# Kernel optimization log

Measured on AMD Instinct MI355X. Metric: run time of the kernel, lower is better.

The kernel has to match this reference:

```python
import jax, jax.numpy as jnp
import numpy as np

B, S, D, H, HG, W, DFF = 2, 4096, 1024, 16, 2, 128, 4096
NEG = -1e30  # stands in for -inf in the original masking (exp underflows to exactly 0)


def _chunk(x, w):
    # overlapping chunks of size 2w with hop w (tf.signal.frame equivalent)
    b, s, d = x.shape
    blocks = x.reshape(b, s // w, w, d)
    return jnp.concatenate([blocks[:, :-1], blocks[:, 1:]], axis=2)  # [b, s//w-1, 2w, d]


def _sliding_scores(q, k, w):
    # q,k: [BH, S, dh] (q pre-scaled). Returns banded scores [BH, S, 2w+1].
    bh, s, d = q.shape
    c = s // w - 1
    attn = jnp.einsum('bcxd,bcyd->bcxy', _chunk(q, w), _chunk(k, w))  # [bh,c,2w,2w]
    # pad one row then reshape: the skew trick from the source (_pad_and_transpose_last_two_dims)
    dca = jnp.pad(attn, ((0, 0), (0, 0), (0, 1), (0, 0))).reshape(bh, c, 2 * w, 2 * w + 1)
    up = jnp.concatenate([dca[:, :, :w, :w + 1], dca[:, -1:, w:, :w + 1]], axis=1)          # [bh,c+1,w,w+1]
    first = jnp.roll(dca, shift=(1, w), axis=(2, 3))[:, :1, :w, :w]                          # first-chunk lower triangle
    low = jnp.concatenate([first, dca[:, :, -(w + 1):-1, w + 1:]], axis=1)                   # [bh,c+1,w,w]
    return jnp.concatenate([low, up], axis=-1).reshape(bh, s, 2 * w + 1)


def _invalid_mask(s, w):
    # _mask_invalid_locations: mask band positions that fall outside [0, S)
    m = jnp.tril(jnp.ones((w, w + 1), jnp.float32))[::-1]
    m = jnp.pad(m, ((0, s - w), (0, w)))
    return (m + m[::-1, ::-1]) > 0  # [s, 2w+1]


def _sliding_value(p, v, w):
    # p: [BH, S, 2w+1] band probs, v: [BH, S, dh] -> [BH, S, dh]
    bh, s, kk = p.shape
    d = v.shape[-1]
    c = s // w
    cp = jnp.pad(p.reshape(bh, c, w, kk), ((0, 0), (0, 0), (0, 0), (0, w + 1)))
    # pad-and-diagonalize skew: row r shifted right by r -> aligns band with 3w value window
    cp = cp.reshape(bh, c, w * (3 * w + 2))[:, :, :-w].reshape(bh, c, w, 3 * w + 1)[:, :, :, :-1]
    pv = jnp.pad(v, ((0, 0), (w, w), (0, 0))).reshape(bh, c + 2, w, d)
    cv = jnp.concatenate([pv[:, :-2], pv[:, 1:-1], pv[:, 2:]], axis=2)  # [bh,c,3w,d]
    return jnp.einsum('bcwk,bckd->bcwd', cp, cv).reshape(bh, s, d)


def _layernorm(x, g, b):
    mu = jnp.mean(x, -1, keepdims=True)
    var = jnp.mean(jnp.square(x - mu), -1, keepdims=True)
    return (x - mu) * jax.lax.rsqrt(var + 1e-6) * g + b


def setup_inputs() -> dict:
    key = jax.random.key(0)
    ks = jax.random.split(key, 8)
    dense = lambda k, i, o: 0.02 * jax.random.normal(k, (i, o), jnp.float32)
    return {
        'x': jax.random.normal(ks[0], (B, S, D), jnp.float32),
        'mask': jnp.zeros((B, 1, 1, S), jnp.float32),
        'wq_k': dense(ks[1], D, D), 'wq_b': jnp.zeros((D,), jnp.float32),
        'wk_k': dense(ks[2], D, D), 'wk_b': jnp.zeros((D,), jnp.float32),
        'wv_k': dense(ks[3], D, D), 'wv_b': jnp.zeros((D,), jnp.float32),
        'wo_k': dense(ks[4], D, D), 'wo_b': jnp.zeros((D,), jnp.float32),
        'ffn_w1': dense(ks[5], D, DFF), 'ffn_b1': jnp.zeros((DFF,), jnp.float32),
        'ffn_w2': dense(ks[6], DFF, D), 'ffn_b2': jnp.zeros((D,), jnp.float32),
        'ln1_g': jnp.ones((D,), jnp.float32), 'ln1_b': jnp.zeros((D,), jnp.float32),
        'ln2_g': jnp.ones((D,), jnp.float32), 'ln2_b': jnp.zeros((D,), jnp.float32),
    }


def reference(x, mask, wq_k, wq_b, wk_k, wk_b, wv_k, wv_b, wo_k, wo_b,
              ffn_w1, ffn_b1, ffn_w2, ffn_b2, ln1_g, ln1_b, ln2_g, ln2_b):
    dh = D // H
    hl = H - HG
    split = lambda t: t.reshape(B, S, H, dh).transpose(0, 2, 1, 3)  # [B,H,S,dh]
    q, k, v = split(x @ wq_k + wq_b), split(x @ wk_k + wk_b), split(x @ wv_k + wv_b)
    scale = 1.0 / jnp.sqrt(jnp.float32(dh))
    # ---- local (sliding-window) heads ----
    ql = (q[:, :hl] * scale).reshape(B * hl, S, dh)
    kl = k[:, :hl].reshape(B * hl, S, dh)
    vl = v[:, :hl].reshape(B * hl, S, dh)
    scores = _sliding_scores(ql, kl, W)
    scores = jnp.where(_invalid_mask(S, W)[None], NEG, scores)
    out_l = _sliding_value(jax.nn.softmax(scores, axis=-1), vl, W).reshape(B, hl, S, dh)
    # ---- global heads (full attention, graph_mask=None branch) ----
    logits = jnp.einsum('bhqd,bhkd->bhqk', q[:, hl:], k[:, hl:]) * scale + mask * (-1000.0)
    out_g = jnp.einsum('bhqk,bhkd->bhqd', jax.nn.softmax(logits, axis=-1), v[:, hl:])
    # ---- merge heads, output proj, residual + LN, FFN (leaky_relu alpha=0.2 = tf default) ----
    attn = jnp.concatenate([out_l, out_g], axis=1).transpose(0, 2, 1, 3).reshape(B, S, D)
    out1 = _layernorm(x + attn @ wo_k + wo_b, ln1_g, ln1_b)
    h = jax.nn.leaky_relu(out1 @ ffn_w1 + ffn_b1, negative_slope=0.2)
    return _layernorm(out1 + h @ ffn_w2 + ffn_b2, ln2_g, ln2_b)
```

## Files before the change

### kernel.cpp

```cpp
#include <hip/hip_runtime.h>
#include <hip/hip_bf16.h>

typedef unsigned short u16;
typedef unsigned int u32;
typedef __attribute__((ext_vector_type(8))) short short8;
typedef __attribute__((ext_vector_type(8))) unsigned short ushort8v;
typedef __attribute__((ext_vector_type(4))) unsigned short ushort4v;
typedef __attribute__((ext_vector_type(4))) float f32x4;

static constexpr int B_ = 2, S_ = 4096, D_ = 1024, H_ = 16, HG_ = 2, W_ = 128, DFF_ = 4096;
static constexpr int HL_ = H_ - HG_;
static constexpr int M_ = B_ * S_;
static constexpr int NCH_ = 4;

static __device__ __forceinline__ u16 f2b(float f) {
    u32 u = __builtin_bit_cast(u32, f);
    u32 r = (u + 0x7fffu + ((u >> 16) & 1u)) >> 16;
    return (u16)r;
}
static __device__ __forceinline__ float b2f(u16 b) {
    return __builtin_bit_cast(float, (u32)b << 16);
}

__global__ __launch_bounds__(256) void k_f32_to_bf16(const float* __restrict__ src,
                                                     u16* __restrict__ dst, int n4) {
    int i = blockIdx.x * 256 + threadIdx.x;
    if (i >= n4) return;
    float4 v = reinterpret_cast<const float4*>(src)[i];
    ushort4v o; o[0] = f2b(v.x); o[1] = f2b(v.y); o[2] = f2b(v.z); o[3] = f2b(v.w);
    reinterpret_cast<ushort4v*>(dst)[i] = o;
}

__global__ __launch_bounds__(256) void k_transpose_bf16(const float* __restrict__ src,
                                                        u16* __restrict__ dst,
                                                        int K, int N, int ro) {
    __shared__ float tile[32][33];
    const int tx = threadIdx.x & 31, ty = threadIdx.x >> 5;
    const int bx = blockIdx.x, by = blockIdx.y;
#pragma unroll
    for (int jj = 0; jj < 4; ++jj) {
        int kk = by * 32 + ty + jj * 8;
        int nn = bx * 32 + tx;
        tile[ty + jj * 8][tx] = src[(size_t)kk * N + nn];
    }
    __syncthreads();
#pragma unroll
    for (int jj = 0; jj < 4; ++jj) {
        int nn = bx * 32 + ty + jj * 8;
        int kk = by * 32 + tx;
        dst[(size_t)(ro + nn) * K + kk] = f2b(tile[tx][ty + jj * 8]);
    }
}

__global__ __launch_bounds__(256) void k_transpose_v(const u16* __restrict__ qkv,
                                                     u16* __restrict__ vT) {
    __shared__ u16 tile[32][33];
    const int tx = threadIdx.x & 31, ty = threadIdx.x >> 5;
    const int s0 = blockIdx.x * 32;
    const int d0 = blockIdx.y * 32;
    const int bh = blockIdx.z;
    const int b = bh >> 4, h = bh & 15;
#pragma unroll
    for (int jj = 0; jj < 4; ++jj) {
        int srow = s0 + ty + jj * 8;
        tile[ty + jj * 8][tx] = qkv[(size_t)(b * S_ + srow) * 3072 + 2048 + h * 64 + d0 + tx];
    }
    __syncthreads();
#pragma unroll
    for (int jj = 0; jj < 4; ++jj) {
        int d = d0 + ty + jj * 8;
        vT[(size_t)((b * H_ + h) * 64 + d) * S_ + s0 + tx] = tile[tx][ty + jj * 8];
    }
}

__global__ void k_pack_bias3(const float* __restrict__ a, const float* __restrict__ b,
                             const float* __restrict__ c, float* __restrict__ dst) {
    int i = blockIdx.x * 256 + threadIdx.x;
    if (i >= 3072) return;
    dst[i] = i < 1024 ? a[i] : (i < 2048 ? b[i - 1024] : c[i - 2048]);
}

#define GLDS16(gp, lp) __builtin_amdgcn_global_load_lds( \
    (const __attribute__((address_space(1))) void*)(gp),  \
    (__attribute__((address_space(3))) void*)(lp), 16, 0, 0)

template <bool LEAKY, bool OUTF, bool OUTB>
__global__ __launch_bounds__(256) void k_gemm(const u16* __restrict__ A, const u16* __restrict__ Bt,
                                              const float* __restrict__ bias,
                                              float* __restrict__ Cf, u16* __restrict__ Cb,
                                              int M, int N, int K) {
    __shared__ __align__(16) u16 lA[128 * 32];
    __shared__ __align__(16) u16 lB[128 * 32];
    const int tid = threadIdx.x;
    const int lane = tid & 63, wave = tid >> 6;
    const int wr = wave >> 1, wc = wave & 1;
    const int m0 = blockIdx.x * 128, n0 = blockIdx.y * 128;

    f32x4 acc[4][4];
#pragma unroll
    for (int i = 0; i < 4; ++i)
#pragma unroll
        for (int j = 0; j < 4; ++j)
#pragma unroll
            for (int e = 0; e < 4; ++e) acc[i][j][e] = 0.f;

    const int arow = tid >> 2;
    const int acol = (tid & 3) * 8;
    const int koff = (lane >> 4) * 8;
    const int rbase = wr * 64 + (lane & 15);
    const int cbase = wc * 64 + (lane & 15);

    for (int k0 = 0; k0 < K; k0 += 32) {
        __syncthreads();
        {
            const u16* ga0 = A + (size_t)(m0 + arow) * K + k0 + acol;
            const u16* ga1 = A + (size_t)(m0 + 64 + arow) * K + k0 + acol;
            GLDS16(ga0, lA + wave * 512);
            GLDS16(ga1, lA + 2048 + wave * 512);
            const u16* gb0 = Bt + (size_t)(n0 + arow) * K + k0 + acol;
            const u16* gb1 = Bt + (size_t)(n0 + 64 + arow) * K + k0 + acol;
            GLDS16(gb0, lB + wave * 512);
            GLDS16(gb1, lB + 2048 + wave * 512);
        }
        __syncthreads();

        short8 af[4], bfr[4];
#pragma unroll
        for (int mi = 0; mi < 4; ++mi)
            af[mi] = *reinterpret_cast<const short8*>(&lA[(rbase + mi * 16) * 32 + koff]);
#pragma unroll
        for (int ni = 0; ni < 4; ++ni)
            bfr[ni] = *reinterpret_cast<const short8*>(&lB[(cbase + ni * 16) * 32 + koff]);
        __builtin_amdgcn_s_setprio(1);
#pragma unroll
        for (int mi = 0; mi < 4; ++mi)
#pragma unroll
            for (int ni = 0; ni < 4; ++ni)
                acc[mi][ni] = __builtin_amdgcn_mfma_f32_16x16x32_bf16(af[mi], bfr[ni], acc[mi][ni], 0, 0, 0);
        __builtin_amdgcn_s_setprio(0);
    }

#pragma unroll
    for (int mi = 0; mi < 4; ++mi) {
        const int rowb = m0 + wr * 64 + mi * 16 + (lane >> 4) * 4;
#pragma unroll
        for (int ni = 0; ni < 4; ++ni) {
            const int col = n0 + wc * 64 + ni * 16 + (lane & 15);
            const float bs = bias[col];
#pragma unroll
            for (int j = 0; j < 4; ++j) {
                float v = acc[mi][ni][j] + bs;
                if (LEAKY) v = v > 0.f ? v : 0.2f * v;
                const size_t idx = (size_t)(rowb + j) * N + col;
                if (OUTF) Cf[idx] = v;
                if (OUTB) Cb[idx] = f2b(v);
            }
        }
    }
}

__global__ __launch_bounds__(256) void k_attn_local(const u16* __restrict__ qkv,
                                                    const u16* __restrict__ vT,
                                                    u16* __restrict__ out) {
    __shared__ __align__(16) u16 Kl[64][72];
    __shared__ __align__(16) u16 Vl[64][72];
    __shared__ __align__(16) u16 Pl[4][1024];
    const int tid = threadIdx.x, lane = tid & 63, wave = tid >> 6;
    const int c = lane & 15, g = lane >> 4;
    const int b = blockIdx.z, h = blockIdx.y;
    const int q0 = blockIdx.x * 64;
    const int qrow = q0 + wave * 16 + c;

    short8 qf[2];
    {
        const u16* qp = qkv + (size_t)(b * S_ + qrow) * 3072 + h * 64 + g * 8;
        qf[0] = *reinterpret_cast<const short8*>(qp);
        qf[1] = *reinterpret_cast<const short8*>(qp + 32);
    }

    f32x4 acc[4];
#pragma unroll
    for (int dt = 0; dt < 4; ++dt)
#pragma unroll
        for (int j = 0; j < 4; ++j) acc[dt][j] = 0.f;
    float mrow = -1e30f, lrow = 0.f;

    const int t_lo = max(0, q0 - W_) >> 6;
    const int t_hi = min(S_ - 1, q0 + 63 + W_) >> 6;
    u16* pw = Pl[wave];

    for (int t = t_lo; t <= t_hi; ++t) {
        __syncthreads();
#pragma unroll
        for (int it = 0; it < 2; ++it) {
            int L = it * 256 + tid;
            int r = L >> 3, cb = (L & 7) * 8;
            *reinterpret_cast<ushort8v*>(&Kl[r][cb]) =
                *reinterpret_cast<const ushort8v*>(&qkv[(size_t)(b * S_ + t * 64 + r) * 3072 + 1024 + h * 64 + cb]);
            *reinterpret_cast<ushort8v*>(&Vl[r][cb]) =
                *reinterpret_cast<const ushort8v*>(&vT[(size_t)((b * H_ + h) * 64 + r) * S_ + t * 64 + cb]);
        }
        __syncthreads();

        f32x4 s[4];
#pragma unroll
        for (int nt = 0; nt < 4; ++nt)
#pragma unroll
            for (int j = 0; j < 4; ++j) s[nt][j] = 0.f;
        __builtin_amdgcn_s_setprio(1);
#pragma unroll
        for (int kc = 0; kc < 2; ++kc) {
#pragma unroll
            for (int nt = 0; nt < 4; ++nt) {
                short8 kf = *reinterpret_cast<const short8*>(&Kl[nt * 16 + c][kc * 32 + g * 8]);
                s[nt] = __builtin_amdgcn_mfma_f32_16x16x32_bf16(kf, qf[kc], s[nt], 0, 0, 0);
            }
        }
        __builtin_amdgcn_s_setprio(0);

        float p[4][4];
        float tmax = -1e30f;
#pragma unroll
        for (int nt = 0; nt < 4; ++nt)
#pragma unroll
            for (int j = 0; j < 4; ++j) {
                float sv = s[nt][j] * 0.125f;
                int key = t * 64 + nt * 16 + 4 * g + j;
                bool val = (key >= qrow - W_) && (key <= qrow + W_);
                sv = val ? sv : -1e30f;
                p[nt][j] = sv;
                tmax = fmaxf(tmax, sv);
            }
        tmax = fmaxf(tmax, __shfl_xor(tmax, 16));
        tmax = fmaxf(tmax, __shfl_xor(tmax, 32));
        float mnew = fmaxf(mrow, tmax);
        float fac = __expf(mrow - mnew);
        mrow = mnew;
        float psum = 0.f;
#pragma unroll
        for (int nt = 0; nt < 4; ++nt)
#pragma unroll
            for (int j = 0; j < 4; ++j) {
                p[nt][j] = __expf(p[nt][j] - mnew);
                psum += p[nt][j];
            }
        lrow = lrow * fac + psum;
#pragma unroll
        for (int dt = 0; dt < 4; ++dt)
#pragma unroll
            for (int j = 0; j < 4; ++j) acc[dt][j] *= fac;

#pragma unroll
        for (int nt = 0; nt < 4; ++nt)
#pragma unroll
            for (int jp = 0; jp < 2; ++jp) {
                u32 pk = (u32)f2b(p[nt][2 * jp]) | ((u32)f2b(p[nt][2 * jp + 1]) << 16);
                int byteoff = (c << 7) + ((nt * 32 + 8 * g + 4 * jp) ^ ((c & 7) << 4));
                *reinterpret_cast<u32*>(reinterpret_cast<char*>(pw) + byteoff) = pk;
            }
        asm volatile("s_waitcnt lgkmcnt(0)" ::: "memory");

        __builtin_amdgcn_s_setprio(1);
#pragma unroll
        for (int h2 = 0; h2 < 2; ++h2) {
            int rb = (c << 7) + ((h2 * 64 + g * 16) ^ ((c & 7) << 4));
            short8 pa = *reinterpret_cast<const short8*>(reinterpret_cast<char*>(pw) + rb);
#pragma unroll
            for (int dt = 0; dt < 4; ++dt) {
                short8 vf = *reinterpret_cast<const short8*>(&Vl[dt * 16 + c][h2 * 32 + g * 8]);
                acc[dt] = __builtin_amdgcn_mfma_f32_16x16x32_bf16(vf, pa, acc[dt], 0, 0, 0);
            }
        }
        __builtin_amdgcn_s_setprio(0);
    }

    float lfull = lrow + __shfl_xor(lrow, 16);
    lfull += __shfl_xor(lfull, 32);
    const float rinv = 1.0f / lfull;

#pragma unroll
    for (int dt = 0; dt < 4; ++dt) {
        u32 w0 = (u32)f2b(acc[dt][0] * rinv) | ((u32)f2b(acc[dt][1] * rinv) << 16);
        u32 w1 = (u32)f2b(acc[dt][2] * rinv) | ((u32)f2b(acc[dt][3] * rinv) << 16);
        uint2 wv; wv.x = w0; wv.y = w1;
        *reinterpret_cast<uint2*>(out + (size_t)(b * S_ + qrow) * 1024 + h * 64 + dt * 16 + 4 * g) = wv;
    }
}

__global__ __launch_bounds__(256) void k_attn_global_part(const u16* __restrict__ qkv,
                                                          const u16* __restrict__ vT,
                                                          const float* __restrict__ mask,
                                                          float* __restrict__ po,
                                                          float* __restrict__ ml) {
    __shared__ __align__(16) u16 Kl[64][72];
    __shared__ __align__(16) u16 Vl[64][72];
    __shared__ __align__(16) u16 Pl[4][1024];
    __shared__ float maskl[64];
    const int tid = threadIdx.x, lane = tid & 63, wave = tid >> 6;
    const int c = lane & 15, g = lane >> 4;
    const int b = blockIdx.z;
    const int hh = blockIdx.y >> 2, ch = blockIdx.y & 3;
    const int h = HL_ + hh;
    const int q0 = blockIdx.x * 64;
    const int qrow = q0 + wave * 16 + c;

    short8 qf[2];
    {
        const u16* qp = qkv + (size_t)(b * S_ + qrow) * 3072 + h * 64 + g * 8;
        qf[0] = *reinterpret_cast<const short8*>(qp);
        qf[1] = *reinterpret_cast<const short8*>(qp + 32);
    }

    f32x4 acc[4];
#pragma unroll
    for (int dt = 0; dt < 4; ++dt)
#pragma unroll
        for (int j = 0; j < 4; ++j) acc[dt][j] = 0.f;
    float mrow = -1e30f, lrow = 0.f;
    u16* pw = Pl[wave];

    const int t_lo = ch * (S_ / 64 / NCH_), t_hi = t_lo + (S_ / 64 / NCH_) - 1;
    for (int t = t_lo; t <= t_hi; ++t) {
        __syncthreads();
#pragma unroll
        for (int it = 0; it < 2; ++it) {
            int L = it * 256 + tid;
            int r = L >> 3, cb = (L & 7) * 8;
            *reinterpret_cast<ushort8v*>(&Kl[r][cb]) =
                *reinterpret_cast<const ushort8v*>(&qkv[(size_t)(b * S_ + t * 64 + r) * 3072 + 1024 + h * 64 + cb]);
            *reinterpret_cast<ushort8v*>(&Vl[r][cb]) =
                *reinterpret_cast<const ushort8v*>(&vT[(size_t)((b * H_ + h) * 64 + r) * S_ + t * 64 + cb]);
        }
        if (tid < 64) maskl[tid] = mask[b * S_ + t * 64 + tid] * (-1000.0f);
        __syncthreads();

        f32x4 s[4];
#pragma unroll
        for (int nt = 0; nt < 4; ++nt)
#pragma unroll
            for (int j = 0; j < 4; ++j) s[nt][j] = 0.f;
        __builtin_amdgcn_s_setprio(1);
#pragma unroll
        for (int kc = 0; kc < 2; ++kc) {
#pragma unroll
            for (int nt = 0; nt < 4; ++nt) {
                short8 kf = *reinterpret_cast<const short8*>(&Kl[nt * 16 + c][kc * 32 + g * 8]);
                s[nt] = __builtin_amdgcn_mfma_f32_16x16x32_bf16(kf, qf[kc], s[nt], 0, 0, 0);
            }
        }
        __builtin_amdgcn_s_setprio(0);

        float p[4][4];
        float tmax = -1e30f;
#pragma unroll
        for (int nt = 0; nt < 4; ++nt)
#pragma unroll
            for (int j = 0; j < 4; ++j) {
                float sv = s[nt][j] * 0.125f + maskl[nt * 16 + 4 * g + j];
                p[nt][j] = sv;
                tmax = fmaxf(tmax, sv);
            }
        tmax = fmaxf(tmax, __shfl_xor(tmax, 16));
        tmax = fmaxf(tmax, __shfl_xor(tmax, 32));
        float mnew = fmaxf(mrow, tmax);
        float fac = __expf(mrow - mnew);
        mrow = mnew;
        float psum = 0.f;
#pragma unroll
        for (int nt = 0; nt < 4; ++nt)
#pragma unroll
            for (int j = 0; j < 4; ++j) {
                p[nt][j] = __expf(p[nt][j] - mnew);
                psum += p[nt][j];
            }
        lrow = lrow * fac + psum;
#pragma unroll
        for (int dt = 0; dt < 4; ++dt)
#pragma unroll
            for (int j = 0; j < 4; ++j) acc[dt][j] *= fac;

#pragma unroll
        for (int nt = 0; nt < 4; ++nt)
#pragma unroll
            for (int jp = 0; jp < 2; ++jp) {
                u32 pk = (u32)f2b(p[nt][2 * jp]) | ((u32)f2b(p[nt][2 * jp + 1]) << 16);
                int byteoff = (c << 7) + ((nt * 32 + 8 * g + 4 * jp) ^ ((c & 7) << 4));
                *reinterpret_cast<u32*>(reinterpret_cast<char*>(pw) + byteoff) = pk;
            }
        asm volatile("s_waitcnt lgkmcnt(0)" ::: "memory");

        __builtin_amdgcn_s_setprio(1);
#pragma unroll
        for (int h2 = 0; h2 < 2; ++h2) {
            int rb = (c << 7) + ((h2 * 64 + g * 16) ^ ((c & 7) << 4));
            short8 pa = *reinterpret_cast<const short8*>(reinterpret_cast<char*>(pw) + rb);
#pragma unroll
            for (int dt = 0; dt < 4; ++dt) {
                short8 vf = *reinterpret_cast<const short8*>(&Vl[dt * 16 + c][h2 * 32 + g * 8]);
                acc[dt] = __builtin_amdgcn_mfma_f32_16x16x32_bf16(vf, pa, acc[dt], 0, 0, 0);
            }
        }
        __builtin_amdgcn_s_setprio(0);
    }

    float lfull = lrow + __shfl_xor(lrow, 16);
    lfull += __shfl_xor(lfull, 32);

    float* po_blk = po + ((((size_t)(b * HG_ + hh) * NCH_ + ch) * (S_ / 64) + blockIdx.x) * 4096);
    const int ql = wave * 16 + c;
#pragma unroll
    for (int dt = 0; dt < 4; ++dt)
        *reinterpret_cast<f32x4*>(po_blk + ql * 64 + dt * 16 + 4 * g) = acc[dt];
    if (g == 0) {
        size_t mb = (((size_t)(b * HG_ + hh) * NCH_ + ch) * S_ + q0 + ql) * 2;
        ml[mb] = mrow;
        ml[mb + 1] = lfull;
    }
}

__global__ __launch_bounds__(256) void k_attn_merge(const float* __restrict__ po,
                                                    const float* __restrict__ ml,
                                                    u16* __restrict__ out) {
    const int qb = blockIdx.x, hh = blockIdx.y, b = blockIdx.z;
    const int t = threadIdx.x;
    const int ql = t >> 2, d0 = (t & 3) * 16;
    const int q = qb * 64 + ql;

    float mv[NCH_], lv[NCH_];
    float M = -1e30f;
#pragma unroll
    for (int ch = 0; ch < NCH_; ++ch) {
        size_t mb = (((size_t)(b * HG_ + hh) * NCH_ + ch) * S_ + q) * 2;
        mv[ch] = ml[mb];
        lv[ch] = ml[mb + 1];
        M = fmaxf(M, mv[ch]);
    }
    float wch[NCH_], L = 0.f;
#pragma unroll
    for (int ch = 0; ch < NCH_; ++ch) {
        wch[ch] = __expf(mv[ch] - M);
        L += wch[ch] * lv[ch];
    }
    const float rL = 1.0f / L;

    float o[16];
#pragma unroll
    for (int i = 0; i < 16; ++i) o[i] = 0.f;
#pragma unroll
    for (int ch = 0; ch < NCH_; ++ch) {
        const float* pb = po + ((((size_t)(b * HG_ + hh) * NCH_ + ch) * (S_ / 64) + qb) * 4096) + ql * 64 + d0;
        const float w = wch[ch];
#pragma unroll
        for (int i = 0; i < 4; ++i) {
            float4 v = reinterpret_cast<const float4*>(pb)[i];
            o[4 * i + 0] += w * v.x; o[4 * i + 1] += w * v.y;
            o[4 * i + 2] += w * v.z; o[4 * i + 3] += w * v.w;
        }
    }
    ushort8v r0, r1;
#pragma unroll
    for (int i = 0; i < 8; ++i) { r0[i] = f2b(o[i] * rL); r1[i] = f2b(o[8 + i] * rL); }
    u16* op = out + (size_t)(b * S_ + q) * 1024 + (HL_ + hh) * 64 + d0;
    *reinterpret_cast<ushort8v*>(op) = r0;
    *reinterpret_cast<ushort8v*>(op + 8) = r1;
}

__global__ __launch_bounds__(256) void k_ln(const float* __restrict__ base, const float* __restrict__ delta,
                                            const float* __restrict__ g, const float* __restrict__ bt,
                                            float* __restrict__ outf, u16* __restrict__ outb) {
    __shared__ float red[8];
    const int row = blockIdx.x, tid = threadIdx.x;
    const int lane = tid & 63, wave = tid >> 6;
    float4 xb = reinterpret_cast<const float4*>(base + (size_t)row * 1024)[tid];
    float4 xd = reinterpret_cast<const float4*>(delta + (size_t)row * 1024)[tid];
    float x0 = xb.x + xd.x, x1 = xb.y + xd.y, x2 = xb.z + xd.z, x3 = xb.w + xd.w;
    float s = x0 + x1 + x2 + x3;
#pragma unroll
    for (int off = 32; off >= 1; off >>= 1) s += __shfl_xor(s, off);
    if (lane == 0) red[wave] = s;
    __syncthreads();
    float mu = (red[0] + red[1] + red[2] + red[3]) * (1.f / 1024.f);
    float d0 = x0 - mu, d1 = x1 - mu, d2 = x2 - mu, d3 = x3 - mu;
    float s2 = d0 * d0 + d1 * d1 + d2 * d2 + d3 * d3;
#pragma unroll
    for (int off = 32; off >= 1; off >>= 1) s2 += __shfl_xor(s2, off);
    if (lane == 0) red[4 + wave] = s2;
    __syncthreads();
    float var = (red[4] + red[5] + red[6] + red[7]) * (1.f / 1024.f);
    float rs = rsqrtf(var + 1e-6f);
    float4 gv = reinterpret_cast<const float4*>(g)[tid];
    float4 bv = reinterpret_cast<const float4*>(bt)[tid];
    float o0 = d0 * rs * gv.x + bv.x;
    float o1 = d1 * rs * gv.y + bv.y;
    float o2 = d2 * rs * gv.z + bv.z;
    float o3 = d3 * rs * gv.w + bv.w;
    if (outf) {
        float4 ov; ov.x = o0; ov.y = o1; ov.z = o2; ov.w = o3;
        reinterpret_cast<float4*>(outf + (size_t)row * 1024)[tid] = ov;
    }
    if (outb) {
        ushort4v ob; ob[0] = f2b(o0); ob[1] = f2b(o1); ob[2] = f2b(o2); ob[3] = f2b(o3);
        reinterpret_cast<ushort4v*>(outb + (size_t)row * 1024)[tid] = ob;
    }
}

extern "C" void kernel_launch(void* const* d_in, const int* in_sizes, int n_in,
                              void* d_out, int out_size, void* d_ws, size_t ws_size,
                              hipStream_t stream) {
    const float* x    = (const float*)d_in[0];
    const float* mask = (const float*)d_in[1];
    const float* wq   = (const float*)d_in[2];
    const float* wq_b = (const float*)d_in[3];
    const float* wk   = (const float*)d_in[4];
    const float* wk_b = (const float*)d_in[5];
    const float* wv   = (const float*)d_in[6];
    const float* wv_b = (const float*)d_in[7];
    const float* wo   = (const float*)d_in[8];
    const float* wo_b = (const float*)d_in[9];
    const float* w1   = (const float*)d_in[10];
    const float* b1   = (const float*)d_in[11];
    const float* w2   = (const float*)d_in[12];
    const float* b2   = (const float*)d_in[13];
    const float* ln1g = (const float*)d_in[14];
    const float* ln1b = (const float*)d_in[15];
    const float* ln2g = (const float*)d_in[16];
    const float* ln2b = (const float*)d_in[17];
    float* out = (float*)d_out;

    char* ws = (char*)d_ws;
    const size_t MB = 1024ull * 1024ull;
    u16*   qkv_b  = (u16*)(ws + 0);
    u16*   h_b    = (u16*)(ws + 0);
    u16*   vTb    = (u16*)(ws + 64 * MB);
    float* ybuf   = (float*)(ws + 64 * MB);
    float* po     = (float*)(ws + 96 * MB);
    float* ml     = (float*)(ws + 113 * MB);
    float* out1   = (float*)(ws + 96 * MB);
    u16*   xb     = (u16*)(ws + 128 * MB);
    u16*   attn_b = (u16*)(ws + 128 * MB);
    u16*   out1_b = (u16*)(ws + 128 * MB);
    u16*   wT     = (u16*)(ws + 144 * MB);
    float* bias3  = (float*)(ws + 152 * MB);

    const dim3 tb(256);

    k_f32_to_bf16<<<(M_ * D_ / 4 + 255) / 256, tb, 0, stream>>>(x, xb, M_ * D_ / 4);
    k_transpose_bf16<<<dim3(32, 32), tb, 0, stream>>>(wq, wT, 1024, 1024, 0);
    k_transpose_bf16<<<dim3(32, 32), tb, 0, stream>>>(wk, wT, 1024, 1024, 1024);
    k_transpose_bf16<<<dim3(32, 32), tb, 0, stream>>>(wv, wT, 1024, 1024, 2048);
    k_pack_bias3<<<12, tb, 0, stream>>>(wq_b, wk_b, wv_b, bias3);
    k_gemm<false, false, true><<<dim3(M_ / 128, 3072 / 128), tb, 0, stream>>>(
        xb, wT, bias3, nullptr, qkv_b, M_, 3072, 1024);
    k_transpose_v<<<dim3(S_ / 32, 2, B_ * H_), tb, 0, stream>>>(qkv_b, vTb);
    k_attn_local<<<dim3(S_ / 64, HL_, B_), tb, 0, stream>>>(qkv_b, vTb, attn_b);
    k_attn_global_part<<<dim3(S_ / 64, HG_ * NCH_, B_), tb, 0, stream>>>(qkv_b, vTb, mask, po, ml);
    k_attn_merge<<<dim3(S_ / 64, HG_, B_), tb, 0, stream>>>(po, ml, attn_b);
    k_transpose_bf16<<<dim3(32, 32), tb, 0, stream>>>(wo, wT, 1024, 1024, 0);
    k_gemm<false, true, false><<<dim3(M_ / 128, 1024 / 128), tb, 0, stream>>>(
        attn_b, wT, wo_b, ybuf, nullptr, M_, 1024, 1024);
    k_ln<<<M_, tb, 0, stream>>>(x, ybuf, ln1g, ln1b, out1, out1_b);
    k_transpose_bf16<<<dim3(128, 32), tb, 0, stream>>>(w1, wT, 1024, 4096, 0);
    k_gemm<true, false, true><<<dim3(M_ / 128, 4096 / 128), tb, 0, stream>>>(
        out1_b, wT, b1, nullptr, h_b, M_, 4096, 1024);
    k_transpose_bf16<<<dim3(32, 128), tb, 0, stream>>>(w2, wT, 4096, 1024, 0);
    k_gemm<false, true, false><<<dim3(M_ / 128, 1024 / 128), tb, 0, stream>>>(
        h_b, wT, b2, ybuf, nullptr, M_, 1024, 4096);
    k_ln<<<M_, tb, 0, stream>>>(out1, ybuf, ln2g, ln2b, out, nullptr);
}
```

Measured before the change: 433.6 us.

## Replace GEMM with 8-wave double-buffered, swizzled, XCD-remapped pipelined kernel

Replaces the 128x128, 4-wave, single-buffered GEMM with an 8-wave kernel using 256-wide N tiles and a 256 or 128 M tile. Global-to-LDS loads for the next K tile are double-buffered and interleaved with MFMA phases using explicit vmcnt waits and barriers. LDS rows use an XOR swizzle to cut bank conflicts, and workgroups are remapped across the 8 XCDs to improve L2 locality. This targets the projection and FFN GEMMs, which dominate runtime, at the cost of more LDS per block and fragile hand-written wait counts.

```diff
diff --git a/kernel.cpp b/kernel.cpp
--- a/kernel.cpp
+++ b/kernel.cpp
@@ -84,79 +84,159 @@
     (const __attribute__((address_space(1))) void*)(gp),  \
     (__attribute__((address_space(3))) void*)(lp), 16, 0, 0)
 
-template <bool LEAKY, bool OUTF, bool OUTB>
-__global__ __launch_bounds__(256) void k_gemm(const u16* __restrict__ A, const u16* __restrict__ Bt,
-                                              const float* __restrict__ bias,
-                                              float* __restrict__ Cf, u16* __restrict__ Cb,
-                                              int M, int N, int K) {
-    __shared__ __align__(16) u16 lA[128 * 32];
-    __shared__ __align__(16) u16 lB[128 * 32];
+template <int N>
+static __device__ __forceinline__ void vwait() {
+    if constexpr (N == 0) asm volatile("s_waitcnt vmcnt(0)" ::: "memory");
+    else if constexpr (N == 3) asm volatile("s_waitcnt vmcnt(3)" ::: "memory");
+    else asm volatile("s_waitcnt vmcnt(4)" ::: "memory");
+    __builtin_amdgcn_sched_barrier(0);
+}
+
+template <int BM, bool LEAKY, bool OUTF, bool OUTB>
+__global__ __launch_bounds__(512, 2) void k_gemm8(const u16* __restrict__ A, const u16* __restrict__ Bt,
+                                                  const float* __restrict__ bias,
+                                                  float* __restrict__ Cf, u16* __restrict__ Cb,
+                                                  int M, int N, int K) {
+    constexpr int MR = BM / 32;
+    constexpr int LA = BM / 128;
+    constexpr int AHALF = BM * 64;
+    constexpr int ABUF = 2 * AHALF;
+    constexpr int BHALF = 16384;
+    constexpr int PARSZ = ABUF + 2 * BHALF;
+    constexpr int NWT = LA + 2;
+
+    __shared__ __align__(16) char smem[2 * PARSZ];
+
     const int tid = threadIdx.x;
-    const int lane = tid & 63, wave = tid >> 6;
-    const int wr = wave >> 1, wc = wave & 1;
-    const int m0 = blockIdx.x * 128, n0 = blockIdx.y * 128;
-
-    f32x4 acc[4][4];
-#pragma unroll
-    for (int i = 0; i < 4; ++i)
+    const int lane = tid & 63, w = tid >> 6;
+    const int wm = w >> 2, wn = w & 3;
+    const int c = lane & 15, g = lane >> 4;
+
+    const int GX = gridDim.x;
+    const int nwg = GX * gridDim.y;
+    const int lin = blockIdx.y * GX + blockIdx.x;
+    const int qq = nwg >> 3, rm = nwg & 7;
+    const int xcd = lin & 7, idx = lin >> 3;
+    const int wg = (xcd < rm ? xcd * (qq + 1) : rm * (qq + 1) + (xcd - rm) * qq) + idx;
+    const int m0 = (wg % GX) * BM;
+    const int n0 = (wg / GX) * 256;
+
+    const int srr = lane >> 2;
+    const int sgc = (lane & 3) ^ ((lane >> 4) & 2);
+    const u16* gA0 = A + (size_t)(m0 + w * 16 + srr) * K + sgc * 8;
+    const u16* gA1 = (LA == 2) ? (A + (size_t)(m0 + 128 + w * 16 + srr) * K + sgc * 8) : gA0;
+    const u16* gB0 = Bt + (size_t)(n0 + w * 16 + srr) * K + sgc * 8;
+    const u16* gB1 = Bt + (size_t)(n0 + 128 + w * 16 + srr) * K + sgc * 8;
+
+#define STG_A(par, kh, kt) do { \
+        char* _d = smem + (par) * PARSZ + (kh) * AHALF + w * 1024; \
+        GLDS16(gA0 + (size_t)(kt) * 64 + (kh) * 32, _d); \
+        if (LA == 2) GLDS16(gA1 + (size_t)(kt) * 64 + (kh) * 32, _d + 8192); \
+    } while (0)
+#define STG_B(par, kh, kt) do { \
+        char* _d = smem + (par) * PARSZ + ABUF + (kh) * BHALF + w * 1024; \
+        GLDS16(gB0 + (size_t)(kt) * 64 + (kh) * 32, _d); \
+        GLDS16(gB1 + (size_t)(kt) * 64 + (kh) * 32, _d + 8192); \
+    } while (0)
+
+    const int gb = (g ^ ((c >> 3) << 1)) * 16;
+    const int arow = c * 64 + gb;
+
+    f32x4 acc[MR][4];
+#pragma unroll
+    for (int i = 0; i < MR; ++i)
 #pragma unroll
         for (int j = 0; j < 4; ++j)
 #pragma unroll
             for (int e = 0; e < 4; ++e) acc[i][j][e] = 0.f;
 
-    const int arow = tid >> 2;
-    const int acol = (tid & 3) * 8;
-    const int koff = (lane >> 4) * 8;
-    const int rbase = wr * 64 + (lane & 15);
-    const int cbase = wc * 64 + (lane & 15);
-
-    for (int k0 = 0; k0 < K; k0 += 32) {
-        __syncthreads();
-        {
-            const u16* ga0 = A + (size_t)(m0 + arow) * K + k0 + acol;
-            const u16* ga1 = A + (size_t)(m0 + 64 + arow) * K + k0 + acol;
-            GLDS16(ga0, lA + wave * 512);
-            GLDS16(ga1, lA + 2048 + wave * 512);
-            const u16* gb0 = Bt + (size_t)(n0 + arow) * K + k0 + acol;
-            const u16* gb1 = Bt + (size_t)(n0 + 64 + arow) * K + k0 + acol;
-            GLDS16(gb0, lB + wave * 512);
-            GLDS16(gb1, lB + 2048 + wave * 512);
-        }
-        __syncthreads();
-
-        short8 af[4], bfr[4];
-#pragma unroll
-        for (int mi = 0; mi < 4; ++mi)
-            af[mi] = *reinterpret_cast<const short8*>(&lA[(rbase + mi * 16) * 32 + koff]);
-#pragma unroll
-        for (int ni = 0; ni < 4; ++ni)
-            bfr[ni] = *reinterpret_cast<const short8*>(&lB[(cbase + ni * 16) * 32 + koff]);
-        __builtin_amdgcn_s_setprio(1);
-#pragma unroll
-        for (int mi = 0; mi < 4; ++mi)
-#pragma unroll
-            for (int ni = 0; ni < 4; ++ni)
-                acc[mi][ni] = __builtin_amdgcn_mfma_f32_16x16x32_bf16(af[mi], bfr[ni], acc[mi][ni], 0, 0, 0);
-        __builtin_amdgcn_s_setprio(0);
-    }
-
-#pragma unroll
-    for (int mi = 0; mi < 4; ++mi) {
-        const int rowb = m0 + wr * 64 + mi * 16 + (lane >> 4) * 4;
+    STG_A(0, 0, 0); STG_B(0, 0, 0); STG_A(0, 1, 0); STG_B(0, 1, 0);
+    vwait<0>();
+    __builtin_amdgcn_s_barrier();
+
+    const int NK = K >> 6;
+    short8 af[MR], b0, b1;
+    for (int kt = 0; kt < NK; ++kt) {
+        const int par = kt & 1, nxt = par ^ 1;
+        const char* bp = smem + par * PARSZ;
+        const bool more = (kt + 1) < NK;
+#pragma unroll
+        for (int mi = 0; mi < MR; ++mi)
+            af[mi] = *reinterpret_cast<const short8*>(bp + (wm * MR + mi) * 1024 + arow);
+        b0 = *reinterpret_cast<const short8*>(bp + ABUF + (wn * 4 + 0) * 1024 + arow);
+        b1 = *reinterpret_cast<const short8*>(bp + ABUF + (wn * 4 + 1) * 1024 + arow);
+        if (more) STG_A(nxt, 0, kt + 1);
+        __builtin_amdgcn_s_barrier();
+        __builtin_amdgcn_s_setprio(1);
+#pragma unroll
+        for (int mi = 0; mi < MR; ++mi) {
+            acc[mi][0] = __builtin_amdgcn_mfma_f32_16x16x32_bf16(af[mi], b0, acc[mi][0], 0, 0, 0);
+            acc[mi][1] = __builtin_amdgcn_mfma_f32_16x16x32_bf16(af[mi], b1, acc[mi][1], 0, 0, 0);
+        }
+        __builtin_amdgcn_s_setprio(0);
+        __builtin_amdgcn_s_barrier();
+        b0 = *reinterpret_cast<const short8*>(bp + ABUF + (wn * 4 + 2) * 1024 + arow);
+        b1 = *reinterpret_cast<const short8*>(bp + ABUF + (wn * 4 + 3) * 1024 + arow);
+        if (more) STG_B(nxt, 0, kt + 1);
+        __builtin_amdgcn_s_barrier();
+        __builtin_amdgcn_s_setprio(1);
+#pragma unroll
+        for (int mi = 0; mi < MR; ++mi) {
+            acc[mi][2] = __builtin_amdgcn_mfma_f32_16x16x32_bf16(af[mi], b0, acc[mi][2], 0, 0, 0);
+            acc[mi][3] = __builtin_amdgcn_mfma_f32_16x16x32_bf16(af[mi], b1, acc[mi][3], 0, 0, 0);
+        }
+        __builtin_amdgcn_s_setprio(0);
+        if (more) vwait<NWT>(); else vwait<0>();
+        __builtin_amdgcn_s_barrier();
+#pragma unroll
+        for (int mi = 0; mi < MR; ++mi)
+            af[mi] = *reinterpret_cast<const short8*>(bp + AHALF + (wm * MR + mi) * 1024 + arow);
+        b0 = *reinterpret_cast<const short8*>(bp + ABUF + BHALF + (wn * 4 + 0) * 1024 + arow);
+        b1 = *reinterpret_cast<const short8*>(bp + ABUF + BHALF + (wn * 4 + 1) * 1024 + arow);
+        if (more) STG_A(nxt, 1, kt + 1);
+        __builtin_amdgcn_s_barrier();
+        __builtin_amdgcn_s_setprio(1);
+#pragma unroll
+        for (int mi = 0; mi < MR; ++mi) {
+            acc[mi][0] = __builtin_amdgcn_mfma_f32_16x16x32_bf16(af[mi], b0, acc[mi][0], 0, 0, 0);
+            acc[mi][1] = __builtin_amdgcn_mfma_f32_16x16x32_bf16(af[mi], b1, acc[mi][1], 0, 0, 0);
+        }
+        __builtin_amdgcn_s_setprio(0);
+        __builtin_amdgcn_s_barrier();
+        b0 = *reinterpret_cast<const short8*>(bp + ABUF + BHALF + (wn * 4 + 2) * 1024 + arow);
+        b1 = *reinterpret_cast<const short8*>(bp + ABUF + BHALF + (wn * 4 + 3) * 1024 + arow);
+        if (more) STG_B(nxt, 1, kt + 1);
+        __builtin_amdgcn_s_barrier();
+        __builtin_amdgcn_s_setprio(1);
+#pragma unroll
+        for (int mi = 0; mi < MR; ++mi) {
+            acc[mi][2] = __builtin_amdgcn_mfma_f32_16x16x32_bf16(af[mi], b0, acc[mi][2], 0, 0, 0);
+            acc[mi][3] = __builtin_amdgcn_mfma_f32_16x16x32_bf16(af[mi], b1, acc[mi][3], 0, 0, 0);
+        }
+        __builtin_amdgcn_s_setprio(0);
+        if (more) vwait<NWT>();
+        __builtin_amdgcn_s_barrier();
+    }
+
+#pragma unroll
+    for (int mi = 0; mi < MR; ++mi) {
+        const int rowb = m0 + wm * (BM / 2) + mi * 16 + g * 4;
 #pragma unroll
         for (int ni = 0; ni < 4; ++ni) {
-            const int col = n0 + wc * 64 + ni * 16 + (lane & 15);
+            const int col = n0 + wn * 64 + ni * 16 + c;
             const float bs = bias[col];
 #pragma unroll
             for (int j = 0; j < 4; ++j) {
                 float v = acc[mi][ni][j] + bs;
                 if (LEAKY) v = v > 0.f ? v : 0.2f * v;
-                const size_t idx = (size_t)(rowb + j) * N + col;
-                if (OUTF) Cf[idx] = v;
-                if (OUTB) Cb[idx] = f2b(v);
-            }
-        }
-    }
+                const size_t idxo = (size_t)(rowb + j) * N + col;
+                if (OUTF) Cf[idxo] = v;
+                if (OUTB) Cb[idxo] = f2b(v);
+            }
+        }
+    }
+#undef STG_A
+#undef STG_B
 }
 
 __global__ __launch_bounds__(256) void k_attn_local(const u16* __restrict__ qkv,
@@ -543,27 +623,28 @@
     float* bias3  = (float*)(ws + 152 * MB);
 
     const dim3 tb(256);
+    const dim3 tg(512);
 
     k_f32_to_bf16<<<(M_ * D_ / 4 + 255) / 256, tb, 0, stream>>>(x, xb, M_ * D_ / 4);
     k_transpose_bf16<<<dim3(32, 32), tb, 0, stream>>>(wq, wT, 1024, 1024, 0);
     k_transpose_bf16<<<dim3(32, 32), tb, 0, stream>>>(wk, wT, 1024, 1024, 1024);
     k_transpose_bf16<<<dim3(32, 32), tb, 0, stream>>>(wv, wT, 1024, 1024, 2048);
     k_pack_bias3<<<12, tb, 0, stream>>>(wq_b, wk_b, wv_b, bias3);
-    k_gemm<false, false, true><<<dim3(M_ / 128, 3072 / 128), tb, 0, stream>>>(
+    k_gemm8<256, false, false, true><<<dim3(M_ / 256, 3072 / 256), tg, 0, stream>>>(
         xb, wT, bias3, nullptr, qkv_b, M_, 3072, 1024);
     k_transpose_v<<<dim3(S_ / 32, 2, B_ * H_), tb, 0, stream>>>(qkv_b, vTb);
     k_attn_local<<<dim3(S_ / 64, HL_, B_), tb, 0, stream>>>(qkv_b, vTb, attn_b);
     k_attn_global_part<<<dim3(S_ / 64, HG_ * NCH_, B_), tb, 0, stream>>>(qkv_b, vTb, mask, po, ml);
     k_attn_merge<<<dim3(S_ / 64, HG_, B_), tb, 0, stream>>>(po, ml, attn_b);
     k_transpose_bf16<<<dim3(32, 32), tb, 0, stream>>>(wo, wT, 1024, 1024, 0);
-    k_gemm<false, true, false><<<dim3(M_ / 128, 1024 / 128), tb, 0, stream>>>(
+    k_gemm8<128, false, true, false><<<dim3(M_ / 128, 1024 / 256), tg, 0, stream>>>(
         attn_b, wT, wo_b, ybuf, nullptr, M_, 1024, 1024);
     k_ln<<<M_, tb, 0, stream>>>(x, ybuf, ln1g, ln1b, out1, out1_b);
     k_transpose_bf16<<<dim3(128, 32), tb, 0, stream>>>(w1, wT, 1024, 4096, 0);
-    k_gemm<true, false, true><<<dim3(M_ / 128, 4096 / 128), tb, 0, stream>>>(
+    k_gemm8<256, true, false, true><<<dim3(M_ / 256, 4096 / 256), tg, 0, stream>>>(
         out1_b, wT, b1, nullptr, h_b, M_, 4096, 1024);
     k_transpose_bf16<<<dim3(32, 128), tb, 0, stream>>>(w2, wT, 4096, 1024, 0);
-    k_gemm<false, true, false><<<dim3(M_ / 128, 1024 / 128), tb, 0, stream>>>(
+    k_gemm8<128, false, true, false><<<dim3(M_ / 128, 1024 / 256), tg, 0, stream>>>(
         h_b, wT, b2, ybuf, nullptr, M_, 1024, 4096);
     k_ln<<<M_, tb, 0, stream>>>(out1, ybuf, ln2g, ln2b, out, nullptr);
 }
```

After: 419.0 us. -3.4%, faster.

## Switch GEMM to 32x32x16 MFMA with XOR-swizzled LDS layout

Applied to the files above, without the earlier changes.

Replaces the 16x16x32 MFMA tiling in the shared GEMM kernel with 32x32x16 MFMA tiles (2x2 per wave), halving the number of LDS fragment loads per k-step. It also XOR-swizzles the 16-byte column groups when staging A and B into LDS to avoid bank conflicts on the new read pattern. The setprio hints are dropped. The epilogue is rewritten to the 32x32 accumulator layout, whose output stores are scattered across rows.

```diff
diff --git a/kernel.cpp b/kernel.cpp
--- a/kernel.cpp
+++ b/kernel.cpp
@@ -7,6 +7,7 @@
 typedef __attribute__((ext_vector_type(8))) unsigned short ushort8v;
 typedef __attribute__((ext_vector_type(4))) unsigned short ushort4v;
 typedef __attribute__((ext_vector_type(4))) float f32x4;
+typedef __attribute__((ext_vector_type(16))) float f32x16;
 
 static constexpr int B_ = 2, S_ = 4096, D_ = 1024, H_ = 16, HG_ = 2, W_ = 128, DFF_ = 4096;
 static constexpr int HL_ = H_ - HG_;
@@ -85,10 +86,10 @@
     (__attribute__((address_space(3))) void*)(lp), 16, 0, 0)
 
 template <bool LEAKY, bool OUTF, bool OUTB>
-__global__ __launch_bounds__(256) void k_gemm(const u16* __restrict__ A, const u16* __restrict__ Bt,
-                                              const float* __restrict__ bias,
-                                              float* __restrict__ Cf, u16* __restrict__ Cb,
-                                              int M, int N, int K) {
+__global__ __launch_bounds__(256) void k_gemm32(const u16* __restrict__ A, const u16* __restrict__ Bt,
+                                                const float* __restrict__ bias,
+                                                float* __restrict__ Cf, u16* __restrict__ Cb,
+                                                int M, int N, int K) {
     __shared__ __align__(16) u16 lA[128 * 32];
     __shared__ __align__(16) u16 lB[128 * 32];
     const int tid = threadIdx.x;
@@ -96,67 +97,69 @@
     const int wr = wave >> 1, wc = wave & 1;
     const int m0 = blockIdx.x * 128, n0 = blockIdx.y * 128;
 
-    f32x4 acc[4][4];
-#pragma unroll
-    for (int i = 0; i < 4; ++i)
-#pragma unroll
-        for (int j = 0; j < 4; ++j)
-#pragma unroll
-            for (int e = 0; e < 4; ++e) acc[i][j][e] = 0.f;
+    f32x16 acc[2][2];
+#pragma unroll
+    for (int i = 0; i < 2; ++i)
+#pragma unroll
+        for (int j = 0; j < 2; ++j)
+#pragma unroll
+            for (int e = 0; e < 16; ++e) acc[i][j][e] = 0.f;
 
     const int arow = tid >> 2;
-    const int acol = (tid & 3) * 8;
-    const int koff = (lane >> 4) * 8;
-    const int rbase = wr * 64 + (lane & 15);
-    const int cbase = wc * 64 + (lane & 15);
+    const int sg = (((tid & 3) ^ (arow & 3))) * 8;
+
+    const int r31 = lane & 31, khi = lane >> 5;
 
     for (int k0 = 0; k0 < K; k0 += 32) {
         __syncthreads();
         {
-            const u16* ga0 = A + (size_t)(m0 + arow) * K + k0 + acol;
-            const u16* ga1 = A + (size_t)(m0 + 64 + arow) * K + k0 + acol;
-            GLDS16(ga0, lA + wave * 512);
-            GLDS16(ga1, lA + 2048 + wave * 512);
-            const u16* gb0 = Bt + (size_t)(n0 + arow) * K + k0 + acol;
-            const u16* gb1 = Bt + (size_t)(n0 + 64 + arow) * K + k0 + acol;
-            GLDS16(gb0, lB + wave * 512);
-            GLDS16(gb1, lB + 2048 + wave * 512);
+            GLDS16(A + (size_t)(m0 + arow) * K + k0 + sg, lA + wave * 512);
+            GLDS16(A + (size_t)(m0 + 64 + arow) * K + k0 + sg, lA + 2048 + wave * 512);
+            GLDS16(Bt + (size_t)(n0 + arow) * K + k0 + sg, lB + wave * 512);
+            GLDS16(Bt + (size_t)(n0 + 64 + arow) * K + k0 + sg, lB + 2048 + wave * 512);
         }
         __syncthreads();
 
-        short8 af[4], bfr[4];
-#pragma unroll
-        for (int mi = 0; mi < 4; ++mi)
-            af[mi] = *reinterpret_cast<const short8*>(&lA[(rbase + mi * 16) * 32 + koff]);
-#pragma unroll
-        for (int ni = 0; ni < 4; ++ni)
-            bfr[ni] = *reinterpret_cast<const short8*>(&lB[(cbase + ni * 16) * 32 + koff]);
-        __builtin_amdgcn_s_setprio(1);
-#pragma unroll
-        for (int mi = 0; mi < 4; ++mi)
-#pragma unroll
-            for (int ni = 0; ni < 4; ++ni)
-                acc[mi][ni] = __builtin_amdgcn_mfma_f32_16x16x32_bf16(af[mi], bfr[ni], acc[mi][ni], 0, 0, 0);
-        __builtin_amdgcn_s_setprio(0);
-    }
-
-#pragma unroll
-    for (int mi = 0; mi < 4; ++mi) {
-        const int rowb = m0 + wr * 64 + mi * 16 + (lane >> 4) * 4;
-#pragma unroll
-        for (int ni = 0; ni < 4; ++ni) {
-            const int col = n0 + wc * 64 + ni * 16 + (lane & 15);
-            const float bs = bias[col];
-#pragma unroll
-            for (int j = 0; j < 4; ++j) {
-                float v = acc[mi][ni][j] + bs;
+#pragma unroll
+        for (int ks = 0; ks < 2; ++ks) {
+            short8 af[2], bf[2];
+#pragma unroll
+            for (int fm = 0; fm < 2; ++fm) {
+                const int row = wr * 64 + fm * 32 + r31;
+                const int byteoff = row * 64 + (((ks * 2 + khi) ^ (row & 3)) << 4);
+                af[fm] = *reinterpret_cast<const short8*>(reinterpret_cast<const char*>(lA) + byteoff);
+            }
+#pragma unroll
+            for (int fn = 0; fn < 2; ++fn) {
+                const int row = wc * 64 + fn * 32 + r31;
+                const int byteoff = row * 64 + (((ks * 2 + khi) ^ (row & 3)) << 4);
+                bf[fn] = *reinterpret_cast<const short8*>(reinterpret_cast<const char*>(lB) + byteoff);
+            }
+#pragma unroll
+            for (int fm = 0; fm < 2; ++fm)
+#pragma unroll
+                for (int fn = 0; fn < 2; ++fn)
+                    acc[fm][fn] = __builtin_amdgcn_mfma_f32_32x32x16_bf16(af[fm], bf[fn], acc[fm][fn], 0, 0, 0);
+        }
+    }
+
+#pragma unroll
+    for (int fm = 0; fm < 2; ++fm)
+#pragma unroll
+        for (int fn = 0; fn < 2; ++fn) {
+            const int colg = n0 + wc * 64 + fn * 32 + r31;
+            const float bs = bias[colg];
+            const int rbase = m0 + wr * 64 + fm * 32 + 4 * khi;
+#pragma unroll
+            for (int r = 0; r < 16; ++r) {
+                const int rowg = rbase + (r & 3) + 8 * (r >> 2);
+                float v = acc[fm][fn][r] + bs;
                 if (LEAKY) v = v > 0.f ? v : 0.2f * v;
-                const size_t idx = (size_t)(rowb + j) * N + col;
-                if (OUTF) Cf[idx] = v;
-                if (OUTB) Cb[idx] = f2b(v);
-            }
-        }
-    }
+                const size_t idxo = (size_t)rowg * N + colg;
+                if (OUTF) Cf[idxo] = v;
+                if (OUTB) Cb[idxo] = f2b(v);
+            }
+        }
 }
 
 __global__ __launch_bounds__(256) void k_attn_local(const u16* __restrict__ qkv,
@@ -549,21 +552,21 @@
     k_transpose_bf16<<<dim3(32, 32), tb, 0, stream>>>(wk, wT, 1024, 1024, 1024);
     k_transpose_bf16<<<dim3(32, 32), tb, 0, stream>>>(wv, wT, 1024, 1024, 2048);
     k_pack_bias3<<<12, tb, 0, stream>>>(wq_b, wk_b, wv_b, bias3);
-    k_gemm<false, false, true><<<dim3(M_ / 128, 3072 / 128), tb, 0, stream>>>(
+    k_gemm32<false, false, true><<<dim3(M_ / 128, 3072 / 128), tb, 0, stream>>>(
         xb, wT, bias3, nullptr, qkv_b, M_, 3072, 1024);
     k_transpose_v<<<dim3(S_ / 32, 2, B_ * H_), tb, 0, stream>>>(qkv_b, vTb);
     k_attn_local<<<dim3(S_ / 64, HL_, B_), tb, 0, stream>>>(qkv_b, vTb, attn_b);
     k_attn_global_part<<<dim3(S_ / 64, HG_ * NCH_, B_), tb, 0, stream>>>(qkv_b, vTb, mask, po, ml);
     k_attn_merge<<<dim3(S_ / 64, HG_, B_), tb, 0, stream>>>(po, ml, attn_b);
     k_transpose_bf16<<<dim3(32, 32), tb, 0, stream>>>(wo, wT, 1024, 1024, 0);
-    k_gemm<false, true, false><<<dim3(M_ / 128, 1024 / 128), tb, 0, stream>>>(
+    k_gemm32<false, true, false><<<dim3(M_ / 128, 1024 / 128), tb, 0, stream>>>(
         attn_b, wT, wo_b, ybuf, nullptr, M_, 1024, 1024);
     k_ln<<<M_, tb, 0, stream>>>(x, ybuf, ln1g, ln1b, out1, out1_b);
     k_transpose_bf16<<<dim3(128, 32), tb, 0, stream>>>(w1, wT, 1024, 4096, 0);
-    k_gemm<true, false, true><<<dim3(M_ / 128, 4096 / 128), tb, 0, stream>>>(
+    k_gemm32<true, false, true><<<dim3(M_ / 128, 4096 / 128), tb, 0, stream>>>(
         out1_b, wT, b1, nullptr, h_b, M_, 4096, 1024);
     k_transpose_bf16<<<dim3(32, 128), tb, 0, stream>>>(w2, wT, 4096, 1024, 0);
-    k_gemm<false, true, false><<<dim3(M_ / 128, 1024 / 128), tb, 0, stream>>>(
+    k_gemm32<false, true, false><<<dim3(M_ / 128, 1024 / 128), tb, 0, stream>>>(
         h_b, wT, b2, ybuf, nullptr, M_, 1024, 4096);
     k_ln<<<M_, tb, 0, stream>>>(out1, ybuf, ln2g, ln2b, out, nullptr);
 }
```

After: 461.7 us. 1.06x slower.

## Triple-buffer GEMM LDS tiles with async global_load_lds prefetch

Applied to the files above, without the earlier changes.

The GEMM k-loop previously loaded each 32-wide K tile into LDS and waited on it before computing. It now keeps three LDS buffers, issues loads three tiles ahead, and uses explicit vmcnt waits so global-to-LDS transfers overlap the MFMA work. This aims to hide memory latency in the projection and FFN GEMMs. In exchange the kernel uses three times the LDS, which may lower occupancy, and it depends on hand-counted waitcnt values being correct.

```diff
diff --git a/kernel.cpp b/kernel.cpp
--- a/kernel.cpp
+++ b/kernel.cpp
@@ -84,13 +84,21 @@
     (const __attribute__((address_space(1))) void*)(gp),  \
     (__attribute__((address_space(3))) void*)(lp), 16, 0, 0)
 
+template <int N>
+static __device__ __forceinline__ void vwait() {
+    if constexpr (N == 0) asm volatile("s_waitcnt vmcnt(0)" ::: "memory");
+    else if constexpr (N == 4) asm volatile("s_waitcnt vmcnt(4)" ::: "memory");
+    else asm volatile("s_waitcnt vmcnt(8)" ::: "memory");
+    __builtin_amdgcn_sched_barrier(0);
+}
+
 template <bool LEAKY, bool OUTF, bool OUTB>
 __global__ __launch_bounds__(256) void k_gemm(const u16* __restrict__ A, const u16* __restrict__ Bt,
                                               const float* __restrict__ bias,
                                               float* __restrict__ Cf, u16* __restrict__ Cb,
                                               int M, int N, int K) {
-    __shared__ __align__(16) u16 lA[128 * 32];
-    __shared__ __align__(16) u16 lB[128 * 32];
+    __shared__ __align__(16) u16 lA[3][128 * 32];
+    __shared__ __align__(16) u16 lB[3][128 * 32];
     const int tid = threadIdx.x;
     const int lane = tid & 63, wave = tid >> 6;
     const int wr = wave >> 1, wc = wave & 1;
@@ -110,27 +118,35 @@
     const int rbase = wr * 64 + (lane & 15);
     const int cbase = wc * 64 + (lane & 15);
 
-    for (int k0 = 0; k0 < K; k0 += 32) {
+    const u16* gA0 = A + (size_t)(m0 + arow) * K + acol;
+    const u16* gA1 = A + (size_t)(m0 + 64 + arow) * K + acol;
+    const u16* gB0 = Bt + (size_t)(n0 + arow) * K + acol;
+    const u16* gB1 = Bt + (size_t)(n0 + 64 + arow) * K + acol;
+
+#define STG(buf, k0) do { \
+        GLDS16(gA0 + (k0), lA[buf] + wave * 512); \
+        GLDS16(gA1 + (k0), lA[buf] + 2048 + wave * 512); \
+        GLDS16(gB0 + (k0), lB[buf] + wave * 512); \
+        GLDS16(gB1 + (k0), lB[buf] + 2048 + wave * 512); \
+    } while (0)
+
+    const int NK = K >> 5;
+    STG(0, 0); STG(1, 32); STG(2, 64);
+
+    int buf = 0;
+    for (int i = 0; i < NK; ++i) {
+        if (i + 2 < NK) vwait<8>();
+        else if (i + 1 < NK) vwait<4>();
+        else vwait<0>();
         __syncthreads();
-        {
-            const u16* ga0 = A + (size_t)(m0 + arow) * K + k0 + acol;
-            const u16* ga1 = A + (size_t)(m0 + 64 + arow) * K + k0 + acol;
-            GLDS16(ga0, lA + wave * 512);
-            GLDS16(ga1, lA + 2048 + wave * 512);
-            const u16* gb0 = Bt + (size_t)(n0 + arow) * K + k0 + acol;
-            const u16* gb1 = Bt + (size_t)(n0 + 64 + arow) * K + k0 + acol;
-            GLDS16(gb0, lB + wave * 512);
-            GLDS16(gb1, lB + 2048 + wave * 512);
-        }
-        __syncthreads();
 
         short8 af[4], bfr[4];
 #pragma unroll
         for (int mi = 0; mi < 4; ++mi)
-            af[mi] = *reinterpret_cast<const short8*>(&lA[(rbase + mi * 16) * 32 + koff]);
+            af[mi] = *reinterpret_cast<const short8*>(&lA[buf][(rbase + mi * 16) * 32 + koff]);
 #pragma unroll
         for (int ni = 0; ni < 4; ++ni)
-            bfr[ni] = *reinterpret_cast<const short8*>(&lB[(cbase + ni * 16) * 32 + koff]);
+            bfr[ni] = *reinterpret_cast<const short8*>(&lB[buf][(cbase + ni * 16) * 32 + koff]);
         __builtin_amdgcn_s_setprio(1);
 #pragma unroll
         for (int mi = 0; mi < 4; ++mi)
@@ -138,6 +154,10 @@
             for (int ni = 0; ni < 4; ++ni)
                 acc[mi][ni] = __builtin_amdgcn_mfma_f32_16x16x32_bf16(af[mi], bfr[ni], acc[mi][ni], 0, 0, 0);
         __builtin_amdgcn_s_setprio(0);
+        __syncthreads();
+
+        if (i + 3 < NK) STG(buf, (i + 3) * 32);
+        buf = buf == 2 ? 0 : buf + 1;
     }
 
 #pragma unroll
@@ -157,6 +177,7 @@
             }
         }
     }
+#undef STG
 }
 
 __global__ __launch_bounds__(256) void k_attn_local(const u16* __restrict__ qkv,
```

Result: faster. 424.7 us (-2.1%).
